# Optimization experiments

Measured on AMD Instinct MI355X. Metric: run time of the kernel, lower is better.

Reference implementation:

```python
import jax, jax.numpy as jnp
import numpy as np

B, QL, DL, RSZ, T = 16, 32, 12, 500, 2
DW, DH = 256, 512
HP = DH // 2  # per-direction GRU hidden
NW, NE = 50000, 100000


def _gru_dir(xp, mask, Wh, bh, reverse):
    # xp: [B, L, 3H'] precomputed input projections; mask: [B, L, 1]
    Hp = Wh.shape[1]
    xp_t = jnp.swapaxes(xp, 0, 1)
    m_t = jnp.swapaxes(mask, 0, 1)
    h0 = jnp.zeros((xp.shape[0], Hp), xp.dtype)

    def step(h, inp):
        x, m = inp
        gh = h @ Wh.T + bh
        r = jax.nn.sigmoid(x[:, :Hp] + gh[:, :Hp])
        z = jax.nn.sigmoid(x[:, Hp:2 * Hp] + gh[:, Hp:2 * Hp])
        n = jnp.tanh(x[:, 2 * Hp:] + r * gh[:, 2 * Hp:])
        hn = (1.0 - z) * n + z * h
        h = m * hn + (1.0 - m) * h  # skip updates at pad tokens
        return h, h

    hT, hs = jax.lax.scan(step, h0, (xp_t, m_t), reverse=reverse)
    return jnp.swapaxes(hs, 0, 1), hT


def _bigru(tokens, emb, Wx, Wh, bx, bh):
    # tokens: [B, L] int, 0 = pad. Wx: [2, 3H', D], Wh: [2, 3H', H'], bx/bh: [2, 3H']
    x = emb[tokens]
    mask = (tokens != 0).astype(x.dtype)[..., None]
    xp_f = jnp.einsum('bld,gd->blg', x, Wx[0]) + bx[0]
    xp_b = jnp.einsum('bld,gd->blg', x, Wx[1]) + bx[1]
    hs_f, hT_f = _gru_dir(xp_f, mask, Wh[0], bh[0], False)
    hs_b, hT_b = _gru_dir(xp_b, mask, Wh[1], bh[1], True)
    word_h = jnp.concatenate([hs_f, hs_b], -1) * mask  # zero pad positions
    sent = jnp.concatenate([hT_f, hT_b], -1)  # last fwd / last bwd hidden
    return word_h, sent


def setup_inputs() -> dict:
    key = jax.random.key(0)
    ks = jax.random.split(key, 12)

    def gru_p(k, din):
        k1, k2 = jax.random.split(k, 2)
        s = 1.0 / float(np.sqrt(HP))
        return (jax.random.normal(k1, (2, 3 * HP, din), jnp.float32) * s,
                jax.random.normal(k2, (2, 3 * HP, HP), jnp.float32) * s,
                jnp.zeros((2, 3 * HP), jnp.float32),
                jnp.zeros((2, 3 * HP), jnp.float32))

    q_Wx, q_Wh, q_bx, q_bh = gru_p(ks[0], DW)
    d_Wx, d_Wh, d_bx, d_bh = gru_p(ks[1], DW)
    kaim = float(np.sqrt(2.0 / DH))
    return {
        'questions': jax.random.randint(ks[2], (B, QL), 0, NW),
        'e_s': jax.random.uniform(ks[3], (B, NE), jnp.float32),
        'pair': jax.random.randint(ks[4], (T, B, RSZ, 2), 0, NE),
        'desc': jax.random.randint(ks[5], (T, B, RSZ, DL), 0, NW),
        'word_emb': jax.random.normal(ks[6], (NW, DW), jnp.float32) * 0.02,
        'q_Wx': q_Wx, 'q_Wh': q_Wh, 'q_bx': q_bx, 'q_bh': q_bh,
        'd_Wx': d_Wx, 'd_Wh': d_Wh, 'd_bx': d_bx, 'd_bh': d_bh,
        'step_W': jax.random.normal(ks[7], (T, DH, DH), jnp.float32) * kaim,
        'step_b': jnp.zeros((T, DH), jnp.float32),
        'rel_W': jax.random.normal(ks[8], (1, DH), jnp.float32) * kaim,
        'rel_b': jnp.zeros((1,), jnp.float32),
        'qcls_W': jax.random.normal(ks[9], (NE, DH), jnp.float32) * kaim,
        'qcls_b': jnp.zeros((NE,), jnp.float32),
    }


def reference(questions, e_s, pair, desc, word_emb, q_Wx, q_Wh, q_bx, q_bh,
              d_Wx, d_Wh, d_bx, d_bh, step_W, step_b, rel_W, rel_b, qcls_W, qcls_b):
    q_word_h, q_emb = _bigru(questions, word_emb, q_Wx, q_Wh, q_bx, q_bh)
    bsz, num_ent = e_s.shape
    last_e = e_s
    for t in range(pair.shape[0]):  # num_steps hops (small, fixed)
        cq = jnp.tanh(q_emb @ step_W[t].T + step_b[t])              # [B,H]
        q_dist = jax.nn.softmax(jnp.einsum('bh,blh->bl', cq, q_word_h), axis=1)
        ctx = jnp.einsum('bl,blh->bh', q_dist, q_word_h)            # [B,H]
        d_tok = desc[t].reshape(-1, desc.shape[-1])                 # [B*rsz, L]
        _, d_emb = _bigru(d_tok, word_emb, d_Wx, d_Wh, d_bx, d_bh)
        d_emb = d_emb.reshape(bsz, -1, d_emb.shape[-1])             # [B,rsz,H]
        d_logit = jnp.einsum('bh,brh,h->br', ctx, d_emb, rel_W[0]) + rel_b[0]
        d_prob = jax.nn.sigmoid(d_logit)                            # [B,rsz]
        sub, obj = pair[t, :, :, 0], pair[t, :, :, 1]
        obj_p = jnp.take_along_axis(last_e, sub, axis=1) * d_prob   # follow: gather
        last_e = jax.vmap(lambda o, p: jnp.zeros((num_ent,), e_s.dtype).at[o].add(p))(obj, obj_p)
        z = jax.lax.stop_gradient(jnp.where(last_e > 1.0, last_e, 1.0))
        last_e = last_e / z
    q_mask = jax.nn.sigmoid(q_emb @ qcls_W.T + qcls_b)
    return last_e * q_mask
```

## Files before the change

### kernel.cpp

```cpp
#include <hip/hip_runtime.h>
#include <math.h>

#define B_    16
#define QL_   32
#define DL_   12
#define RSZ_  500
#define T_    2
#define DW_   256
#define DH_   512
#define HP_   256
#define NW_   50000
#define NE_   100000
#define NSEQD (T_*B_*RSZ_)

typedef _Float16 half8 __attribute__((ext_vector_type(8)));
typedef float   floatx4 __attribute__((ext_vector_type(4)));

__device__ __forceinline__ float sigf(float x){
  return __builtin_amdgcn_rcpf(1.0f + __expf(-x));
}
__device__ __forceinline__ float tanhfast(float x){
  return 1.0f - 2.0f*__builtin_amdgcn_rcpf(1.0f + __expf(2.0f*x));
}

__global__ void k_prep_desc(const float* __restrict__ Wx, const float* __restrict__ Wh,
                            _Float16* __restrict__ Bd) {
  int i = blockIdx.x*256 + threadIdx.x;
  int dir = i / 393216;
  int rem = i % 393216;
  float v;
  if (rem < 262144) {
    int n = rem >> 9, k = rem & 511;
    v = (k < 256) ? Wx[(dir*768 + n)*256 + k] : Wh[(dir*768 + n)*256 + (k-256)];
  } else if (rem < 327680) {
    int r2 = rem - 262144; int j = r2 >> 8, k = r2 & 255;
    v = Wx[(dir*768 + 512 + j)*256 + k];
  } else {
    int r2 = rem - 327680; int j = r2 >> 8, k = r2 & 255;
    v = Wh[(dir*768 + 512 + j)*256 + k];
  }
  Bd[i] = (_Float16)v;
}

__global__ void k_prep_qwh(const float* __restrict__ Wh, _Float16* __restrict__ WhQ) {
  int i = blockIdx.x*256 + threadIdx.x;
  WhQ[i] = (_Float16)Wh[i];
}

__global__ __launch_bounds__(256) void k_xproj(
    const int* __restrict__ questions, const float* __restrict__ emb,
    const float* __restrict__ Wx, const float* __restrict__ bx,
    float* __restrict__ xp)
{
  int b = blockIdx.x, n0 = blockIdx.y*128, dir = blockIdx.z;
  int tid = threadIdx.x;
  __shared__ float As[32*256];
  {
    int l = tid >> 3, c8 = tid & 7;
    int tk = questions[b*QL_ + l];
    const float4* src = (const float4*)(emb + (size_t)tk*256) + c8*8;
    float4* dst = (float4*)(As + l*256 + c8*32);
    #pragma unroll
    for (int q = 0; q < 8; ++q) dst[q] = src[q];
  }
  __syncthreads();
  int rr = tid >> 7, jj = tid & 127;
  int n = n0 + jj;
  const float4* W4 = (const float4*)(Wx + ((size_t)dir*768 + n)*256);
  const float4* A4 = (const float4*)As;
  float acc[16];
  #pragma unroll
  for (int i = 0; i < 16; ++i) acc[i] = 0.f;
  for (int k4 = 0; k4 < 64; ++k4) {
    float4 wv = W4[k4];
    #pragma unroll
    for (int i = 0; i < 16; ++i) {
      float4 av = A4[(rr*16 + i)*64 + k4];
      acc[i] += av.x*wv.x + av.y*wv.y + av.z*wv.z + av.w*wv.w;
    }
  }
  float bias = bx[dir*768 + n];
  for (int i = 0; i < 16; ++i) {
    int l = rr*16 + i;
    xp[(((size_t)dir*QL_ + l)*16 + b)*768 + n] = acc[i] + bias;
  }
}

__global__ __launch_bounds__(1024, 4) void k_qgru(
    const int* __restrict__ questions, const _Float16* __restrict__ WhQ,
    const float* __restrict__ bh, const float* __restrict__ xp,
    float* __restrict__ qwh, float* __restrict__ qemb)
{
  const int dir = blockIdx.x;
  const int tid = threadIdx.x;
  const int lane = tid & 63, w = tid >> 6;
  const int lm = lane & 15, lq = lane >> 4;
  const int jl = w*16 + lm;

  __shared__ _Float16 hA[16*256];
  __shared__ float xpL[2][16*768];
  __shared__ int tokS[512];

  if (tid < 512) {
    tokS[tid] = questions[tid];
    int row = tid >> 5, c = tid & 31;
    half8 z8 = {0,0,0,0,0,0,0,0};
    *(half8*)(hA + row*256 + (c ^ row)*8) = z8;
  }

  const _Float16* pR = WhQ + ((size_t)dir*768 + jl)*256;
  const _Float16* pZ = WhQ + ((size_t)dir*768 + 256 + jl)*256;
  const _Float16* pG = WhQ + ((size_t)dir*768 + 512 + jl)*256;
  const float bh_r = bh[dir*768 + jl];
  const float bh_z = bh[dir*768 + 256 + jl];
  const float bh_n = bh[dir*768 + 512 + jl];
  float hreg[4] = {0.f,0.f,0.f,0.f};

  for (int t = 0; t < QL_; ++t) {
    int l = dir ? (QL_-1-t) : t;
    int par = t & 1;
    {
      const float4* src = (const float4*)(xp + (((size_t)dir*QL_ + l)*16)*768);
      float4* dst = (float4*)xpL[par];
      dst[tid]        = src[tid];
      dst[tid + 1024] = src[tid + 1024];
      dst[tid + 2048] = src[tid + 2048];
    }
    __syncthreads();

    floatx4 aR = {0,0,0,0}, aZ = {0,0,0,0}, aG = {0,0,0,0};
    #pragma unroll
    for (int kf = 0; kf < 8; ++kf) {
      int p = (kf*4 + lq) ^ lm;
      half8 a = *(const half8*)(hA + lm*256 + p*8);
      int k0 = kf*32 + lq*8;
      half8 br = *(const half8*)(pR + k0);
      half8 bz = *(const half8*)(pZ + k0);
      half8 bg = *(const half8*)(pG + k0);
      aR = __builtin_amdgcn_mfma_f32_16x16x32_f16(a, br, aR, 0,0,0);
      aZ = __builtin_amdgcn_mfma_f32_16x16x32_f16(a, bz, aZ, 0,0,0);
      aG = __builtin_amdgcn_mfma_f32_16x16x32_f16(a, bg, aG, 0,0,0);
    }
    __syncthreads();

    #pragma unroll
    for (int reg = 0; reg < 4; ++reg) {
      int b = lq*4 + reg;
      const float* xb = &xpL[par][b*768];
      float r  = sigf(xb[jl]       + aR[reg] + bh_r);
      float z  = sigf(xb[256 + jl] + aZ[reg] + bh_z);
      float nt = tanhfast(xb[512 + jl] + r*(aG[reg] + bh_n));
      float hold = hreg[reg];
      float hn = (1.f - z)*nt + z*hold;
      int tk = tokS[b*QL_ + l];
      float hnew = (tk != 0) ? hn : hold;
      hreg[reg] = hnew;
      int p2 = (jl >> 3) ^ b;
      hA[b*256 + p2*8 + (jl & 7)] = (_Float16)hnew;
      qwh[((size_t)b*QL_ + l)*512 + dir*256 + jl] = (tk != 0) ? hnew : 0.f;
    }
  }
  #pragma unroll
  for (int reg = 0; reg < 4; ++reg) {
    int b = lq*4 + reg;
    qemb[b*512 + dir*256 + jl] = hreg[reg];
  }
}

__global__ __launch_bounds__(1024, 4) void k_desc_gru(
    const int* __restrict__ desc, const float* __restrict__ emb,
    const _Float16* __restrict__ Bd, const float* __restrict__ bx,
    const float* __restrict__ bh, float* __restrict__ dh)
{
  const int dir  = blockIdx.z;
  const int seq0 = blockIdx.x * 64;
  const int tid  = threadIdx.x;
  const int lane = tid & 63, w = tid >> 6;
  const int lm = lane & 15, lq = lane >> 4;
  const int j0 = w * 16;

  __shared__ _Float16 A2[64*512];
  __shared__ int tokL[2][64];

  {
    int row = tid >> 4, cc = tid & 15;
    half8 z8 = {0,0,0,0,0,0,0,0};
    #pragma unroll
    for (int q = 0; q < 2; ++q) {
      int c = 32 + cc*2 + q;
      *(half8*)(A2 + row*512 + (c ^ row)*8) = z8;
    }
  }

  const int l0 = dir ? (DL_-1) : 0;
  const int dl = dir ? -1 : 1;

  auto stage_x = [&](int ll, int par) {
    int row = tid >> 4, cc = tid & 15;
    int s = seq0 + row;
    int tk = desc[(size_t)s*DL_ + ll];
    if (cc == 0) tokL[par][row] = tk;
    const float4* src = (const float4*)(emb + (size_t)tk*256);
    #pragma unroll
    for (int q = 0; q < 2; ++q) {
      int c = cc*2 + q;
      float4 v0 = src[c*2], v1 = src[c*2+1];
      half8 hv;
      hv[0]=(_Float16)v0.x; hv[1]=(_Float16)v0.y; hv[2]=(_Float16)v0.z; hv[3]=(_Float16)v0.w;
      hv[4]=(_Float16)v1.x; hv[5]=(_Float16)v1.y; hv[6]=(_Float16)v1.z; hv[7]=(_Float16)v1.w;
      *(half8*)(A2 + row*512 + (c ^ row)*8) = hv;
    }
  };
  stage_x(l0, 0);

  const _Float16* Bdir = Bd + (size_t)dir * 393216;
  const int jl = j0 + lm;
  const _Float16* pR = Bdir + (size_t)jl*512;
  const _Float16* pZ = Bdir + (size_t)(256 + jl)*512;
  const _Float16* pX = Bdir + 262144 + (size_t)jl*256;
  const _Float16* pG = Bdir + 327680 + (size_t)jl*256;

  const float bias_r = bx[dir*768 + jl]       + bh[dir*768 + jl];
  const float bias_z = bx[dir*768 + 256 + jl] + bh[dir*768 + 256 + jl];
  const float bias_n = bx[dir*768 + 512 + jl];
  const float bias_g = bh[dir*768 + 512 + jl];

  int l = l0;
  for (int t = 0; t < DL_; ++t, l += dl) {
    __syncthreads();

    floatx4 accR[4], accZ[4], accN[4], accG[4];
    #pragma unroll
    for (int mi = 0; mi < 4; ++mi) {
      floatx4 z4 = {0.f,0.f,0.f,0.f};
      accR[mi]=z4; accZ[mi]=z4; accN[mi]=z4; accG[mi]=z4;
    }

    #pragma unroll
    for (int half = 0; half < 2; ++half) {
      #pragma unroll 4
      for (int kk = 0; kk < 8; ++kk) {
        int kfx = half*8 + kk;
        int k0 = kfx*32 + lq*8;
        half8 br = *(const half8*)(pR + k0);
        half8 bz = *(const half8*)(pZ + k0);
        half8 bb = half ? *(const half8*)(pG + (k0 - 256))
                        : *(const half8*)(pX + k0);
        int cb = kfx*4 + lq;
        #pragma unroll
        for (int mi = 0; mi < 4; ++mi) {
          int row = mi*16 + lm;
          half8 a = *(const half8*)(A2 + row*512 + (cb ^ row)*8);
          accR[mi] = __builtin_amdgcn_mfma_f32_16x16x32_f16(a, br, accR[mi], 0,0,0);
          accZ[mi] = __builtin_amdgcn_mfma_f32_16x16x32_f16(a, bz, accZ[mi], 0,0,0);
          if (half) accG[mi] = __builtin_amdgcn_mfma_f32_16x16x32_f16(a, bb, accG[mi], 0,0,0);
          else      accN[mi] = __builtin_amdgcn_mfma_f32_16x16x32_f16(a, bb, accN[mi], 0,0,0);
        }
      }
    }

    __syncthreads();

    int par = t & 1;
    #pragma unroll
    for (int mi = 0; mi < 4; ++mi) {
      #pragma unroll
      for (int reg = 0; reg < 4; ++reg) {
        int m = mi*16 + lq*4 + reg;
        float r  = sigf(accR[mi][reg] + bias_r);
        float z  = sigf(accZ[mi][reg] + bias_z);
        float nt = tanhfast(accN[mi][reg] + bias_n + r*(accG[mi][reg] + bias_g));
        int c2 = 32 + (jl >> 3);
        _Float16* hp = A2 + m*512 + ((c2 ^ m)*8) + (jl & 7);
        float hold = (float)(*hp);
        float hn = (1.f - z)*nt + z*hold;
        int tk = tokL[par][m];
        float hnew = (tk != 0) ? hn : hold;
        *hp = (_Float16)hnew;
        if (t == DL_-1)
          dh[((size_t)dir*NSEQD + seq0 + m)*256 + jl] = hnew;
      }
    }
    if (t < DL_-1) stage_x(l + dl, (t+1) & 1);
  }
}

__global__ __launch_bounds__(256) void k_attn(
    const float* __restrict__ qemb, const float* __restrict__ qwh,
    const float* __restrict__ sW, const float* __restrict__ sb,
    const float* __restrict__ relW, float* __restrict__ u, int t)
{
  int b = blockIdx.x, tid = threadIdx.x;
  __shared__ float qe[512];
  __shared__ float cq[512];
  __shared__ float lg[32];
  __shared__ float dist[32];
  qe[tid]     = qemb[b*512 + tid];
  qe[tid+256] = qemb[b*512 + 256 + tid];
  __syncthreads();
  const float4* qe4 = (const float4*)qe;
  for (int nn = 0; nn < 2; ++nn) {
    int n = tid + nn*256;
    const float4* w4 = (const float4*)(sW + ((size_t)t*512 + n)*512);
    float acc = 0.f;
    for (int k4 = 0; k4 < 128; ++k4) {
      float4 w = w4[k4]; float4 q = qe4[k4];
      acc += w.x*q.x + w.y*q.y + w.z*q.z + w.w*q.w;
    }
    cq[n] = tanhfast(acc + sb[t*512 + n]);
  }
  __syncthreads();
  if (tid < 32) {
    const float4* r4 = (const float4*)(qwh + ((size_t)b*QL_ + tid)*512);
    const float4* c4 = (const float4*)cq;
    float acc = 0.f;
    for (int k4 = 0; k4 < 128; ++k4) {
// ... 48 lines not shown
                          const float* __restrict__ esrc, float* __restrict__ edst,
                          int t, int clampflag)
{
  int o = blockIdx.x*256 + threadIdx.x;
  if (o >= B_*RSZ_) return;
  int b = o / RSZ_, r = o % RSZ_;
  const int* pp = pair + (((size_t)t*B_ + b)*RSZ_ + r)*2;
  int sub = pp[0], obj = pp[1];
  float v = esrc[(size_t)b*NE_ + sub];
  if (clampflag) v = fminf(v, 1.0f);
  atomicAdd(edst + (size_t)b*NE_ + obj, v * dprob[o]);
}

__global__ __launch_bounds__(256) void k_final(
    const float* __restrict__ qemb, const float* __restrict__ W,
    const float* __restrict__ bias, const float* __restrict__ efin,
    float* __restrict__ out)
{
  int tid = threadIdx.x;
  int lane = tid & 63;
  int ks = lane & 15, bg = lane >> 4;
  int b = (tid >> 6)*4 + bg;
  float q[32];
  {
    const float4* q4 = (const float4*)(qemb + b*512 + ks*32);
    #pragma unroll
    for (int i = 0; i < 8; ++i) {
      float4 v = q4[i];
      q[4*i]=v.x; q[4*i+1]=v.y; q[4*i+2]=v.z; q[4*i+3]=v.w;
    }
  }
  int e0 = blockIdx.x*256;
  int eend = (e0+256 < NE_) ? e0+256 : NE_;
  for (int e = e0; e < eend; ++e) {
    const float4* w4 = (const float4*)(W + (size_t)e*512 + ks*32);
    float acc = 0.f;
    #pragma unroll
    for (int i = 0; i < 8; ++i) {
      float4 v = w4[i];
      acc += v.x*q[4*i] + v.y*q[4*i+1] + v.z*q[4*i+2] + v.w*q[4*i+3];
    }
    acc += __shfl_xor(acc, 1);
    acc += __shfl_xor(acc, 2);
    acc += __shfl_xor(acc, 4);
    acc += __shfl_xor(acc, 8);
    if (ks == 0) {
      float msk = sigf(acc + bias[e]);
      float ev = fminf(efin[(size_t)b*NE_ + e], 1.0f);
      out[(size_t)b*NE_ + e] = ev * msk;
    }
  }
}

extern "C" void kernel_launch(void* const* d_in, const int* in_sizes, int n_in,
                              void* d_out, int out_size, void* d_ws, size_t ws_size,
                              hipStream_t stream)
{
  const int*   questions = (const int*)d_in[0];
  const float* e_s   = (const float*)d_in[1];
  const int*   pair  = (const int*)d_in[2];
  const int*   desc  = (const int*)d_in[3];
  const float* emb   = (const float*)d_in[4];
  const float* qWx   = (const float*)d_in[5];
  const float* qWh   = (const float*)d_in[6];
  const float* qbx   = (const float*)d_in[7];
  const float* qbh   = (const float*)d_in[8];
  const float* dWx   = (const float*)d_in[9];
  const float* dWh   = (const float*)d_in[10];
  const float* dbx   = (const float*)d_in[11];
  const float* dbh   = (const float*)d_in[12];
  const float* stepW = (const float*)d_in[13];
  const float* stepb = (const float*)d_in[14];
  const float* relW  = (const float*)d_in[15];
  const float* relb  = (const float*)d_in[16];
  const float* qclsW = (const float*)d_in[17];
  const float* qclsb = (const float*)d_in[18];
  float* out = (float*)d_out;

  char* ws = (char*)d_ws;
  size_t off = 0;
  auto alloc = [&](size_t bytes)->void* {
    void* p = ws + off; off += (bytes + 255) & ~(size_t)255; return p;
  };
  _Float16* Bd   = (_Float16*)alloc((size_t)2*393216*sizeof(_Float16));
  _Float16* WhQ  = (_Float16*)alloc((size_t)2*768*256*sizeof(_Float16));
  float* xp   = (float*)alloc((size_t)2*QL_*16*768*sizeof(float));
  float* qemb = (float*)alloc((size_t)16*512*sizeof(float));
  float* qwh  = (float*)alloc((size_t)16*QL_*512*sizeof(float));
  float* dh   = (float*)alloc((size_t)2*NSEQD*256*sizeof(float));
  float* u    = (float*)alloc((size_t)16*512*sizeof(float));
  float* dprob= (float*)alloc((size_t)B_*RSZ_*sizeof(float));
  float* ebuf = (float*)alloc((size_t)2*B_*NE_*sizeof(float));

  hipMemsetAsync(ebuf, 0, (size_t)2*B_*NE_*sizeof(float), stream);

  k_prep_desc<<<3072, 256, 0, stream>>>(dWx, dWh, Bd);
  k_prep_qwh<<<1536, 256, 0, stream>>>(qWh, WhQ);

  k_xproj<<<dim3(16,6,2), 256, 0, stream>>>(questions, emb, qWx, qbx, xp);
  k_qgru<<<2, 1024, 0, stream>>>(questions, WhQ, qbh, xp, qwh, qemb);

  k_desc_gru<<<dim3(250,1,2), 1024, 0, stream>>>(desc, emb, Bd, dbx, dbh, dh);

  for (int t = 0; t < T_; ++t) {
    k_attn<<<16, 256, 0, stream>>>(qemb, qwh, stepW, stepb, relW, u, t);
    k_dlogit<<<2000, 256, 0, stream>>>(u, dh, relb, dprob, t);
    const float* esrc = (t == 0) ? e_s : ebuf;
    float* edst = ebuf + (size_t)t*B_*NE_;
    k_scatter<<<32, 256, 0, stream>>>(pair, dprob, esrc, edst, t, t);
  }
  k_final<<<(NE_+255)/256, 256, 0, stream>>>(qemb, qclsW, qclsb, ebuf + (size_t)B_*NE_, out);
}
```

Measured before the change: 1.821 ms.

## Fuse question and description GRUs into one launch with register-resident weights

Merges the question GRU and description GRU into a single kernel launch: 250 blocks handle description sequences (now 128 rows per block) and 2 extra blocks run the question GRU concurrently. GRU weight fragments are preloaded into registers instead of being re-read from global memory each step. The embedding table is pre-converted to fp16 once so description gathers move half the bytes, and the next step's input tokens are prefetched in registers. The entity buffer now aliases the fp16 embedding scratch and is zeroed after the fused kernel. The trade-off is very high register pressure (weights plus 32 accumulators per thread) and an extra conversion pass over the 50k×256 embedding table.

```diff
diff --git a/kernel.cpp b/kernel.cpp
--- a/kernel.cpp
+++ b/kernel.cpp
@@ -12,6 +12,9 @@
 #define NW_   50000
 #define NE_   100000
 #define NSEQD (T_*B_*RSZ_)
+#define MDESC 128
+#define NBLK_DESC 250
+#define NBLK_FUSED 252
 
 typedef _Float16 half8 __attribute__((ext_vector_type(8)));
 typedef float   floatx4 __attribute__((ext_vector_type(4)));
@@ -47,6 +50,16 @@
   WhQ[i] = (_Float16)Wh[i];
 }
 
+__global__ void k_prep_emb16(const float* __restrict__ emb, _Float16* __restrict__ emb16) {
+  int i = blockIdx.x*256 + threadIdx.x;
+  const float4* s = (const float4*)emb + (size_t)i*2;
+  float4 a = s[0], b = s[1];
+  half8 h;
+  h[0]=(_Float16)a.x; h[1]=(_Float16)a.y; h[2]=(_Float16)a.z; h[3]=(_Float16)a.w;
+  h[4]=(_Float16)b.x; h[5]=(_Float16)b.y; h[6]=(_Float16)b.z; h[7]=(_Float16)b.w;
+  *(half8*)(emb16 + (size_t)i*8) = h;
+}
+
 __global__ __launch_bounds__(256) void k_xproj(
     const int* __restrict__ questions, const float* __restrict__ emb,
     const float* __restrict__ Wx, const float* __restrict__ bx,
@@ -86,202 +99,208 @@
   }
 }
 
-__global__ __launch_bounds__(1024, 4) void k_qgru(
+__global__ __launch_bounds__(1024) void k_fused(
+    const int* __restrict__ desc, const _Float16* __restrict__ emb16,
+    const _Float16* __restrict__ Bd, const float* __restrict__ dbx,
+    const float* __restrict__ dbh, float* __restrict__ dh,
     const int* __restrict__ questions, const _Float16* __restrict__ WhQ,
-    const float* __restrict__ bh, const float* __restrict__ xp,
+    const float* __restrict__ qbh, const float* __restrict__ xp,
     float* __restrict__ qwh, float* __restrict__ qemb)
 {
-  const int dir = blockIdx.x;
+  __shared__ __align__(16) char smem[137216];
+  const int bid = blockIdx.x;
   const int tid = threadIdx.x;
   const int lane = tid & 63, w = tid >> 6;
   const int lm = lane & 15, lq = lane >> 4;
   const int jl = w*16 + lm;
 
-  __shared__ _Float16 hA[16*256];
-  __shared__ float xpL[2][16*768];
-  __shared__ int tokS[512];
-
-  if (tid < 512) {
-    tokS[tid] = questions[tid];
-    int row = tid >> 5, c = tid & 31;
-    half8 z8 = {0,0,0,0,0,0,0,0};
-    *(half8*)(hA + row*256 + (c ^ row)*8) = z8;
-  }
-
-  const _Float16* pR = WhQ + ((size_t)dir*768 + jl)*256;
-  const _Float16* pZ = WhQ + ((size_t)dir*768 + 256 + jl)*256;
-  const _Float16* pG = WhQ + ((size_t)dir*768 + 512 + jl)*256;
-  const float bh_r = bh[dir*768 + jl];
-  const float bh_z = bh[dir*768 + 256 + jl];
-  const float bh_n = bh[dir*768 + 512 + jl];
-  float hreg[4] = {0.f,0.f,0.f,0.f};
-
-  for (int t = 0; t < QL_; ++t) {
-    int l = dir ? (QL_-1-t) : t;
-    int par = t & 1;
+  if (bid < NBLK_DESC) {
+    const int dir  = (bid >= 125) ? 1 : 0;
+    const int seq0 = (bid - dir*125) * MDESC;
+    _Float16* A2   = (_Float16*)smem;
+    int*      tokA = (int*)(smem + MDESC*512*2);
+
+    for (int i = tid; i < MDESC*DL_; i += 1024)
+      tokA[i] = desc[(size_t)seq0*DL_ + i];
+
+    const int srow = tid >> 3, sp = tid & 7;
     {
-      const float4* src = (const float4*)(xp + (((size_t)dir*QL_ + l)*16)*768);
-      float4* dst = (float4*)xpL[par];
+      half8 z8 = {0,0,0,0,0,0,0,0};
+      #pragma unroll
+      for (int q = 0; q < 4; ++q) {
+        int c = 32 + sp*4 + q;
+        *(half8*)(A2 + srow*512 + ((c ^ (srow & 63))*8)) = z8;
+      }
+    }
+
+    const _Float16* Bdir = Bd + (size_t)dir*393216;
+    const _Float16* pR = Bdir + (size_t)jl*512 + lq*8;
+    const _Float16* pZ = Bdir + (size_t)(256 + jl)*512 + lq*8;
+    const _Float16* pX = Bdir + 262144 + (size_t)jl*256 + lq*8;
+    const _Float16* pG = Bdir + 327680 + (size_t)jl*256 + lq*8;
+    half8 bR[16], bZ[16], bX[8], bG[8];
+    #pragma unroll
+    for (int kt = 0; kt < 16; ++kt) {
+      bR[kt] = *(const half8*)(pR + kt*32);
+      bZ[kt] = *(const half8*)(pZ + kt*32);
+    }
+    #pragma unroll
+    for (int kt = 0; kt < 8; ++kt) {
+      bX[kt] = *(const half8*)(pX + kt*32);
+      bG[kt] = *(const half8*)(pG + kt*32);
+    }
+
+    const float bias_r = dbx[dir*768 + jl]       + dbh[dir*768 + jl];
+    const float bias_z = dbx[dir*768 + 256 + jl] + dbh[dir*768 + 256 + jl];
+    const float bias_n = dbx[dir*768 + 512 + jl];
+    const float bias_g = dbh[dir*768 + 512 + jl];
+
+    const int l0 = dir ? (DL_-1) : 0;
+    const int dl = dir ? -1 : 1;
+
+    half8 P[4];
+    auto ldx = [&](int ll) {
+      int tk = desc[(size_t)(seq0 + srow)*DL_ + ll];
+      const half8* src = (const half8*)(emb16 + (size_t)tk*256) + sp*4;
+      #pragma unroll
+      for (int q = 0; q < 4; ++q) P[q] = src[q];
+    };
+    auto stw = [&]() {
+      #pragma unroll
+      for (int q = 0; q < 4; ++q) {
+        int c = sp*4 + q;
+        *(half8*)(A2 + srow*512 + ((c ^ (srow & 63))*8)) = P[q];
+      }
+    };
+    ldx(l0); stw();
+    ldx(l0 + dl);
+    __syncthreads();
+
+    int l = l0;
+    for (int t = 0; t < DL_; ++t, l += dl) {
+      floatx4 accR[8], accZ[8], accN[8], accG[8];
+      #pragma unroll
+      for (int mi = 0; mi < 8; ++mi) {
+        floatx4 z4 = {0.f,0.f,0.f,0.f};
+        accR[mi]=z4; accZ[mi]=z4; accN[mi]=z4; accG[mi]=z4;
+      }
+      #pragma unroll
+      for (int kt = 0; kt < 16; ++kt) {
+        #pragma unroll
+        for (int mi = 0; mi < 8; ++mi) {
+          int row = mi*16 + lm;
+          half8 a = *(const half8*)(A2 + row*512 + (((kt*4 + lq) ^ (row & 63))*8));
+          accR[mi] = __builtin_amdgcn_mfma_f32_16x16x32_f16(a, bR[kt], accR[mi], 0,0,0);
+          accZ[mi] = __builtin_amdgcn_mfma_f32_16x16x32_f16(a, bZ[kt], accZ[mi], 0,0,0);
+          if (kt < 8) accN[mi] = __builtin_amdgcn_mfma_f32_16x16x32_f16(a, bX[kt],   accN[mi], 0,0,0);
+          else        accG[mi] = __builtin_amdgcn_mfma_f32_16x16x32_f16(a, bG[kt-8], accG[mi], 0,0,0);
+        }
+      }
+      __syncthreads();
+
+      #pragma unroll
+      for (int mi = 0; mi < 8; ++mi) {
+        #pragma unroll
+        for (int reg = 0; reg < 4; ++reg) {
+          int m = mi*16 + lq*4 + reg;
+          float r  = sigf(accR[mi][reg] + bias_r);
+          float z  = sigf(accZ[mi][reg] + bias_z);
+          float nt = tanhfast(accN[mi][reg] + bias_n + r*(accG[mi][reg] + bias_g));
+          int c2 = 32 + (jl >> 3);
+          _Float16* hp = A2 + m*512 + ((c2 ^ (m & 63))*8) + (jl & 7);
+          float hold = (float)(*hp);
+          float hn = (1.f - z)*nt + z*hold;
+          int tk = tokA[m*DL_ + l];
+          float hnew = (tk != 0) ? hn : hold;
+          *hp = (_Float16)hnew;
+          if (t == DL_-1)
+            dh[((size_t)dir*NSEQD + seq0 + m)*256 + jl] = hnew;
+        }
+      }
+      if (t < DL_-1) {
+        stw();
+        if (t < DL_-2) ldx(l + 2*dl);
+      }
+      __syncthreads();
+    }
+  } else {
+    const int dir = bid - NBLK_DESC;
+    _Float16* hA   = (_Float16*)smem;
+    float*    xpL  = (float*)(smem + 8192);
+    int*      tokS = (int*)(smem + 8192 + 98304);
+
+    if (tid < 512) {
+      tokS[tid] = questions[tid];
+      int row = tid >> 5, c = tid & 31;
+      half8 z8 = {0,0,0,0,0,0,0,0};
+      *(half8*)(hA + row*256 + ((c ^ row)*8)) = z8;
+    }
+
+    const _Float16* qpR = WhQ + ((size_t)dir*768 + jl)*256 + lq*8;
+    const _Float16* qpZ = WhQ + ((size_t)dir*768 + 256 + jl)*256 + lq*8;
+    const _Float16* qpG = WhQ + ((size_t)dir*768 + 512 + jl)*256 + lq*8;
+    half8 bQR[8], bQZ[8], bQG[8];
+    #pragma unroll
+    for (int kf = 0; kf < 8; ++kf) {
+      bQR[kf] = *(const half8*)(qpR + kf*32);
+      bQZ[kf] = *(const half8*)(qpZ + kf*32);
+      bQG[kf] = *(const half8*)(qpG + kf*32);
+    }
+    const float bh_r = qbh[dir*768 + jl];
+    const float bh_z = qbh[dir*768 + 256 + jl];
+    const float bh_n = qbh[dir*768 + 512 + jl];
+    float hreg[4] = {0.f,0.f,0.f,0.f};
+
+    auto stq = [&](int ll, int par) {
+      const float4* src = (const float4*)(xp + (((size_t)dir*QL_ + ll)*16)*768);
+      float4* dst = (float4*)(xpL + par*12288);
       dst[tid]        = src[tid];
       dst[tid + 1024] = src[tid + 1024];
       dst[tid + 2048] = src[tid + 2048];
-    }
+    };
+    stq(dir ? QL_-1 : 0, 0);
     __syncthreads();
 
-    floatx4 aR = {0,0,0,0}, aZ = {0,0,0,0}, aG = {0,0,0,0};
-    #pragma unroll
-    for (int kf = 0; kf < 8; ++kf) {
-      int p = (kf*4 + lq) ^ lm;
-      half8 a = *(const half8*)(hA + lm*256 + p*8);
-      int k0 = kf*32 + lq*8;
-      half8 br = *(const half8*)(pR + k0);
-      half8 bz = *(const half8*)(pZ + k0);
-      half8 bg = *(const half8*)(pG + k0);
-      aR = __builtin_amdgcn_mfma_f32_16x16x32_f16(a, br, aR, 0,0,0);
-      aZ = __builtin_amdgcn_mfma_f32_16x16x32_f16(a, bz, aZ, 0,0,0);
-      aG = __builtin_amdgcn_mfma_f32_16x16x32_f16(a, bg, aG, 0,0,0);
-    }
-    __syncthreads();
-
+    for (int t = 0; t < QL_; ++t) {
+      int l = dir ? (QL_-1-t) : t;
+      int par = t & 1;
+      if (t < QL_-1) stq(dir ? (QL_-2-t) : (t+1), par ^ 1);
+
+      floatx4 aR = {0,0,0,0}, aZ = {0,0,0,0}, aG = {0,0,0,0};
+      #pragma unroll
+      for (int kf = 0; kf < 8; ++kf) {
+        int p = (kf*4 + lq) ^ lm;
+        half8 a = *(const half8*)(hA + lm*256 + p*8);
+        aR = __builtin_amdgcn_mfma_f32_16x16x32_f16(a, bQR[kf], aR, 0,0,0);
+        aZ = __builtin_amdgcn_mfma_f32_16x16x32_f16(a, bQZ[kf], aZ, 0,0,0);
+        aG = __builtin_amdgcn_mfma_f32_16x16x32_f16(a, bQG[kf], aG, 0,0,0);
+      }
+      __syncthreads();
+
+      const float* xb0 = xpL + par*12288;
+      #pragma unroll
+      for (int reg = 0; reg < 4; ++reg) {
+        int b = lq*4 + reg;
+        const float* xb = xb0 + b*768;
+        float r  = sigf(xb[jl]       + aR[reg] + bh_r);
+        float z  = sigf(xb[256 + jl] + aZ[reg] + bh_z);
+        float nt = tanhfast(xb[512 + jl] + r*(aG[reg] + bh_n));
+        float hold = hreg[reg];
+        float hn = (1.f - z)*nt + z*hold;
+        int tk = tokS[b*QL_ + l];
+        float hnew = (tk != 0) ? hn : hold;
+        hreg[reg] = hnew;
+        int p2 = (jl >> 3) ^ b;
+        hA[b*256 + p2*8 + (jl & 7)] = (_Float16)hnew;
+        qwh[((size_t)b*QL_ + l)*512 + dir*256 + jl] = (tk != 0) ? hnew : 0.f;
+      }
+      __syncthreads();
+    }
     #pragma unroll
     for (int reg = 0; reg < 4; ++reg) {
       int b = lq*4 + reg;
-      const float* xb = &xpL[par][b*768];
-      float r  = sigf(xb[jl]       + aR[reg] + bh_r);
-      float z  = sigf(xb[256 + jl] + aZ[reg] + bh_z);
-      float nt = tanhfast(xb[512 + jl] + r*(aG[reg] + bh_n));
-      float hold = hreg[reg];
-      float hn = (1.f - z)*nt + z*hold;
-      int tk = tokS[b*QL_ + l];
-      float hnew = (tk != 0) ? hn : hold;
-      hreg[reg] = hnew;
-      int p2 = (jl >> 3) ^ b;
-      hA[b*256 + p2*8 + (jl & 7)] = (_Float16)hnew;
-      qwh[((size_t)b*QL_ + l)*512 + dir*256 + jl] = (tk != 0) ? hnew : 0.f;
-    }
-  }
-  #pragma unroll
-  for (int reg = 0; reg < 4; ++reg) {
-    int b = lq*4 + reg;
-    qemb[b*512 + dir*256 + jl] = hreg[reg];
-  }
-}
-
-__global__ __launch_bounds__(1024, 4) void k_desc_gru(
-    const int* __restrict__ desc, const float* __restrict__ emb,
-    const _Float16* __restrict__ Bd, const float* __restrict__ bx,
-    const float* __restrict__ bh, float* __restrict__ dh)
-{
-  const int dir  = blockIdx.z;
-  const int seq0 = blockIdx.x * 64;
-  const int tid  = threadIdx.x;
-  const int lane = tid & 63, w = tid >> 6;
-  const int lm = lane & 15, lq = lane >> 4;
-  const int j0 = w * 16;
-
-  __shared__ _Float16 A2[64*512];
-  __shared__ int tokL[2][64];
-
-  {
-    int row = tid >> 4, cc = tid & 15;
-    half8 z8 = {0,0,0,0,0,0,0,0};
-    #pragma unroll
-    for (int q = 0; q < 2; ++q) {
-      int c = 32 + cc*2 + q;
-      *(half8*)(A2 + row*512 + (c ^ row)*8) = z8;
-    }
-  }
-
-  const int l0 = dir ? (DL_-1) : 0;
-  const int dl = dir ? -1 : 1;
-
-  auto stage_x = [&](int ll, int par) {
-    int row = tid >> 4, cc = tid & 15;
-    int s = seq0 + row;
-    int tk = desc[(size_t)s*DL_ + ll];
-    if (cc == 0) tokL[par][row] = tk;
-    const float4* src = (const float4*)(emb + (size_t)tk*256);
-    #pragma unroll
-    for (int q = 0; q < 2; ++q) {
-      int c = cc*2 + q;
-      float4 v0 = src[c*2], v1 = src[c*2+1];
-      half8 hv;
-      hv[0]=(_Float16)v0.x; hv[1]=(_Float16)v0.y; hv[2]=(_Float16)v0.z; hv[3]=(_Float16)v0.w;
-      hv[4]=(_Float16)v1.x; hv[5]=(_Float16)v1.y; hv[6]=(_Float16)v1.z; hv[7]=(_Float16)v1.w;
-      *(half8*)(A2 + row*512 + (c ^ row)*8) = hv;
-    }
-  };
-  stage_x(l0, 0);
-
-  const _Float16* Bdir = Bd + (size_t)dir * 393216;
-  const int jl = j0 + lm;
-  const _Float16* pR = Bdir + (size_t)jl*512;
-  const _Float16* pZ = Bdir + (size_t)(256 + jl)*512;
-  const _Float16* pX = Bdir + 262144 + (size_t)jl*256;
-  const _Float16* pG = Bdir + 327680 + (size_t)jl*256;
-
-  const float bias_r = bx[dir*768 + jl]       + bh[dir*768 + jl];
-  const float bias_z = bx[dir*768 + 256 + jl] + bh[dir*768 + 256 + jl];
-  const float bias_n = bx[dir*768 + 512 + jl];
-  const float bias_g = bh[dir*768 + 512 + jl];
-
-  int l = l0;
-  for (int t = 0; t < DL_; ++t, l += dl) {
-    __syncthreads();
-
-    floatx4 accR[4], accZ[4], accN[4], accG[4];
-    #pragma unroll
-    for (int mi = 0; mi < 4; ++mi) {
-      floatx4 z4 = {0.f,0.f,0.f,0.f};
-      accR[mi]=z4; accZ[mi]=z4; accN[mi]=z4; accG[mi]=z4;
-    }
-
-    #pragma unroll
-    for (int half = 0; half < 2; ++half) {
-      #pragma unroll 4
-      for (int kk = 0; kk < 8; ++kk) {
-        int kfx = half*8 + kk;
-        int k0 = kfx*32 + lq*8;
-        half8 br = *(const half8*)(pR + k0);
-        half8 bz = *(const half8*)(pZ + k0);
-        half8 bb = half ? *(const half8*)(pG + (k0 - 256))
-                        : *(const half8*)(pX + k0);
-        int cb = kfx*4 + lq;
-        #pragma unroll
-        for (int mi = 0; mi < 4; ++mi) {
-          int row = mi*16 + lm;
-          half8 a = *(const half8*)(A2 + row*512 + (cb ^ row)*8);
-          accR[mi] = __builtin_amdgcn_mfma_f32_16x16x32_f16(a, br, accR[mi], 0,0,0);
-          accZ[mi] = __builtin_amdgcn_mfma_f32_16x16x32_f16(a, bz, accZ[mi], 0,0,0);
-          if (half) accG[mi] = __builtin_amdgcn_mfma_f32_16x16x32_f16(a, bb, accG[mi], 0,0,0);
-          else      accN[mi] = __builtin_amdgcn_mfma_f32_16x16x32_f16(a, bb, accN[mi], 0,0,0);
-        }
-      }
-    }
-
-    __syncthreads();
-
-    int par = t & 1;
-    #pragma unroll
-    for (int mi = 0; mi < 4; ++mi) {
-      #pragma unroll
-      for (int reg = 0; reg < 4; ++reg) {
-        int m = mi*16 + lq*4 + reg;
-        float r  = sigf(accR[mi][reg] + bias_r);
-        float z  = sigf(accZ[mi][reg] + bias_z);
-        float nt = tanhfast(accN[mi][reg] + bias_n + r*(accG[mi][reg] + bias_g));
-        int c2 = 32 + (jl >> 3);
-        _Float16* hp = A2 + m*512 + ((c2 ^ m)*8) + (jl & 7);
-        float hold = (float)(*hp);
-        float hn = (1.f - z)*nt + z*hold;
-        int tk = tokL[par][m];
-        float hnew = (tk != 0) ? hn : hold;
-        *hp = (_Float16)hnew;
-        if (t == DL_-1)
-          dh[((size_t)dir*NSEQD + seq0 + m)*256 + jl] = hnew;
-      }
-    }
-    if (t < DL_-1) stage_x(l + dl, (t+1) & 1);
+      qemb[b*512 + dir*256 + jl] = hreg[reg];
+    }
   }
 }
 
@@ -448,23 +467,25 @@
   };
   _Float16* Bd   = (_Float16*)alloc((size_t)2*393216*sizeof(_Float16));
   _Float16* WhQ  = (_Float16*)alloc((size_t)2*768*256*sizeof(_Float16));
+  _Float16* emb16= (_Float16*)alloc((size_t)NW_*256*sizeof(_Float16));
   float* xp   = (float*)alloc((size_t)2*QL_*16*768*sizeof(float));
   float* qemb = (float*)alloc((size_t)16*512*sizeof(float));
   float* qwh  = (float*)alloc((size_t)16*QL_*512*sizeof(float));
   float* dh   = (float*)alloc((size_t)2*NSEQD*256*sizeof(float));
   float* u    = (float*)alloc((size_t)16*512*sizeof(float));
   float* dprob= (float*)alloc((size_t)B_*RSZ_*sizeof(float));
-  float* ebuf = (float*)alloc((size_t)2*B_*NE_*sizeof(float));
-
-  hipMemsetAsync(ebuf, 0, (size_t)2*B_*NE_*sizeof(float), stream);
+  float* ebuf = (float*)emb16;
 
   k_prep_desc<<<3072, 256, 0, stream>>>(dWx, dWh, Bd);
   k_prep_qwh<<<1536, 256, 0, stream>>>(qWh, WhQ);
+  k_prep_emb16<<<6250, 256, 0, stream>>>(emb, emb16);
 
   k_xproj<<<dim3(16,6,2), 256, 0, stream>>>(questions, emb, qWx, qbx, xp);
-  k_qgru<<<2, 1024, 0, stream>>>(questions, WhQ, qbh, xp, qwh, qemb);
-
-  k_desc_gru<<<dim3(250,1,2), 1024, 0, stream>>>(desc, emb, Bd, dbx, dbh, dh);
+
+  k_fused<<<NBLK_FUSED, 1024, 0, stream>>>(desc, emb16, Bd, dbx, dbh, dh,
+                                           questions, WhQ, qbh, xp, qwh, qemb);
+
+  hipMemsetAsync(ebuf, 0, (size_t)2*B_*NE_*sizeof(float), stream);
 
   for (int t = 0; t < T_; ++t) {
     k_attn<<<16, 256, 0, stream>>>(qemb, qwh, stepW, stepb, relW, u, t);
```

New measurement: 2.461 ms. 35.1% more time.

## Fuse question and description GRUs into one launch with fp16 embedding table

Applied to the files above, without the earlier changes.

Merges the question GRU (2 blocks) and the description GRU (500 blocks) into a single kernel, so the long serial question recurrence overlaps the description work instead of running alone. The embedding table is pre-converted to fp16 once, which halves gather traffic, and the next token's embeddings are register-prefetched one step ahead. Token ids are staged in LDS up front, the question xp tile is read straight from global memory instead of through LDS, and the entity buffer aliases the fp16 table and is zeroed afterwards. The final kernel is also unrolled by two entities. The extra conversion pass over the full 50k-row table adds traffic that may offset the savings.

```diff
diff --git a/kernel.cpp b/kernel.cpp
--- a/kernel.cpp
+++ b/kernel.cpp
@@ -12,6 +12,9 @@
 #define NW_   50000
 #define NE_   100000
 #define NSEQD (T_*B_*RSZ_)
+#define MDESC 64
+#define NBLK_DESC 500
+#define NBLK_FUSED 502
 
 typedef _Float16 half8 __attribute__((ext_vector_type(8)));
 typedef float   floatx4 __attribute__((ext_vector_type(4)));
@@ -47,6 +50,16 @@
   WhQ[i] = (_Float16)Wh[i];
 }
 
+__global__ void k_prep_emb16(const float* __restrict__ emb, _Float16* __restrict__ emb16) {
+  int i = blockIdx.x*256 + threadIdx.x;
+  const float4* s = (const float4*)emb + (size_t)i*2;
+  float4 a = s[0], b = s[1];
+  half8 h;
+  h[0]=(_Float16)a.x; h[1]=(_Float16)a.y; h[2]=(_Float16)a.z; h[3]=(_Float16)a.w;
+  h[4]=(_Float16)b.x; h[5]=(_Float16)b.y; h[6]=(_Float16)b.z; h[7]=(_Float16)b.w;
+  *(half8*)(emb16 + (size_t)i*8) = h;
+}
+
 __global__ __launch_bounds__(256) void k_xproj(
     const int* __restrict__ questions, const float* __restrict__ emb,
     const float* __restrict__ Wx, const float* __restrict__ bx,
@@ -86,202 +99,204 @@
   }
 }
 
-__global__ __launch_bounds__(1024, 4) void k_qgru(
+__global__ __launch_bounds__(1024, 4) void k_fused(
+    const int* __restrict__ desc, const _Float16* __restrict__ emb16,
+    const _Float16* __restrict__ Bd, const float* __restrict__ dbx,
+    const float* __restrict__ dbh, float* __restrict__ dh,
     const int* __restrict__ questions, const _Float16* __restrict__ WhQ,
-    const float* __restrict__ bh, const float* __restrict__ xp,
+    const float* __restrict__ qbh, const float* __restrict__ xp,
     float* __restrict__ qwh, float* __restrict__ qemb)
 {
-  const int dir = blockIdx.x;
+  __shared__ __align__(16) char smem[68608];
+  const int bid = blockIdx.x;
   const int tid = threadIdx.x;
   const int lane = tid & 63, w = tid >> 6;
   const int lm = lane & 15, lq = lane >> 4;
   const int jl = w*16 + lm;
 
-  __shared__ _Float16 hA[16*256];
-  __shared__ float xpL[2][16*768];
-  __shared__ int tokS[512];
-
-  if (tid < 512) {
-    tokS[tid] = questions[tid];
-    int row = tid >> 5, c = tid & 31;
-    half8 z8 = {0,0,0,0,0,0,0,0};
-    *(half8*)(hA + row*256 + (c ^ row)*8) = z8;
-  }
-
-  const _Float16* pR = WhQ + ((size_t)dir*768 + jl)*256;
-  const _Float16* pZ = WhQ + ((size_t)dir*768 + 256 + jl)*256;
-  const _Float16* pG = WhQ + ((size_t)dir*768 + 512 + jl)*256;
-  const float bh_r = bh[dir*768 + jl];
-  const float bh_z = bh[dir*768 + 256 + jl];
-  const float bh_n = bh[dir*768 + 512 + jl];
-  float hreg[4] = {0.f,0.f,0.f,0.f};
-
-  for (int t = 0; t < QL_; ++t) {
-    int l = dir ? (QL_-1-t) : t;
-    int par = t & 1;
+  if (bid < NBLK_DESC) {
+    const int dir  = (bid >= 250) ? 1 : 0;
+    const int seq0 = (bid - dir*250) * MDESC;
+    _Float16* A2   = (_Float16*)smem;
+    int*      tokA = (int*)(smem + MDESC*512*2);
+
+    if (tid < MDESC*DL_)
+      tokA[tid] = desc[(size_t)seq0*DL_ + tid];
+
     {
-      const float4* src = (const float4*)(xp + (((size_t)dir*QL_ + l)*16)*768);
-      float4* dst = (float4*)xpL[par];
-      dst[tid]        = src[tid];
-      dst[tid + 1024] = src[tid + 1024];
-      dst[tid + 2048] = src[tid + 2048];
+      int row = tid >> 4, cc = tid & 15;
+      half8 z8 = {0,0,0,0,0,0,0,0};
+      #pragma unroll
+      for (int q = 0; q < 2; ++q) {
+        int c = 32 + cc*2 + q;
+        *(half8*)(A2 + row*512 + ((c ^ row)*8)) = z8;
+      }
     }
     __syncthreads();
 
-    floatx4 aR = {0,0,0,0}, aZ = {0,0,0,0}, aG = {0,0,0,0};
-    #pragma unroll
-    for (int kf = 0; kf < 8; ++kf) {
-      int p = (kf*4 + lq) ^ lm;
-      half8 a = *(const half8*)(hA + lm*256 + p*8);
-      int k0 = kf*32 + lq*8;
-      half8 br = *(const half8*)(pR + k0);
-      half8 bz = *(const half8*)(pZ + k0);
-      half8 bg = *(const half8*)(pG + k0);
-      aR = __builtin_amdgcn_mfma_f32_16x16x32_f16(a, br, aR, 0,0,0);
-      aZ = __builtin_amdgcn_mfma_f32_16x16x32_f16(a, bz, aZ, 0,0,0);
-      aG = __builtin_amdgcn_mfma_f32_16x16x32_f16(a, bg, aG, 0,0,0);
-    }
+    const _Float16* Bdir = Bd + (size_t)dir * 393216;
+    const _Float16* pR = Bdir + (size_t)jl*512;
+    const _Float16* pZ = Bdir + (size_t)(256 + jl)*512;
+    const _Float16* pX = Bdir + 262144 + (size_t)jl*256;
+    const _Float16* pG = Bdir + 327680 + (size_t)jl*256;
+
+    const float bias_r = dbx[dir*768 + jl]       + dbh[dir*768 + jl];
+    const float bias_z = dbx[dir*768 + 256 + jl] + dbh[dir*768 + 256 + jl];
+    const float bias_n = dbx[dir*768 + 512 + jl];
+    const float bias_g = dbh[dir*768 + 512 + jl];
+
+    const int l0 = dir ? (DL_-1) : 0;
+    const int dl = dir ? -1 : 1;
+
+    const int srow = tid >> 4, sp = tid & 15;
+    half8 P[2];
+    auto ldx = [&](int ll) {
+      int tk = tokA[srow*DL_ + ll];
+      const half8* src = (const half8*)(emb16 + (size_t)tk*256) + sp*2;
+      P[0] = __builtin_nontemporal_load(src);
+      P[1] = __builtin_nontemporal_load(src + 1);
+    };
+    auto stw = [&]() {
+      #pragma unroll
+      for (int q = 0; q < 2; ++q) {
+        int c = sp*2 + q;
+        *(half8*)(A2 + srow*512 + ((c ^ srow)*8)) = P[q];
+      }
+    };
+    ldx(l0); stw();
+    ldx(l0 + dl);
     __syncthreads();
 
+    int l = l0;
+    for (int t = 0; t < DL_; ++t, l += dl) {
+      floatx4 accR[4], accZ[4], accN[4], accG[4];
+      #pragma unroll
+      for (int mi = 0; mi < 4; ++mi) {
+        floatx4 z4 = {0.f,0.f,0.f,0.f};
+        accR[mi]=z4; accZ[mi]=z4; accN[mi]=z4; accG[mi]=z4;
+      }
+
+      #pragma unroll
+      for (int half = 0; half < 2; ++half) {
+        #pragma unroll 4
+        for (int kk = 0; kk < 8; ++kk) {
+          int kfx = half*8 + kk;
+          int k0 = kfx*32 + lq*8;
+          half8 br = *(const half8*)(pR + k0);
+          half8 bz = *(const half8*)(pZ + k0);
+          half8 bb = half ? *(const half8*)(pG + (k0 - 256))
+                          : *(const half8*)(pX + k0);
+          int cb = kfx*4 + lq;
+          #pragma unroll
+          for (int mi = 0; mi < 4; ++mi) {
+            int row = mi*16 + lm;
+            half8 a = *(const half8*)(A2 + row*512 + ((cb ^ row)*8));
+            accR[mi] = __builtin_amdgcn_mfma_f32_16x16x32_f16(a, br, accR[mi], 0,0,0);
+            accZ[mi] = __builtin_amdgcn_mfma_f32_16x16x32_f16(a, bz, accZ[mi], 0,0,0);
+            if (half) accG[mi] = __builtin_amdgcn_mfma_f32_16x16x32_f16(a, bb, accG[mi], 0,0,0);
+            else      accN[mi] = __builtin_amdgcn_mfma_f32_16x16x32_f16(a, bb, accN[mi], 0,0,0);
+          }
+        }
+      }
+
+      __syncthreads();
+
+      #pragma unroll
+      for (int mi = 0; mi < 4; ++mi) {
+        #pragma unroll
+        for (int reg = 0; reg < 4; ++reg) {
+          int m = mi*16 + lq*4 + reg;
+          float r  = sigf(accR[mi][reg] + bias_r);
+          float z  = sigf(accZ[mi][reg] + bias_z);
+          float nt = tanhfast(accN[mi][reg] + bias_n + r*(accG[mi][reg] + bias_g));
+          int c2 = 32 + (jl >> 3);
+          _Float16* hp = A2 + m*512 + ((c2 ^ m)*8) + (jl & 7);
+          float hold = (float)(*hp);
+          float hn = (1.f - z)*nt + z*hold;
+          int tk = tokA[m*DL_ + l];
+          float hnew = (tk != 0) ? hn : hold;
+          *hp = (_Float16)hnew;
+          if (t == DL_-1)
+            dh[((size_t)dir*NSEQD + seq0 + m)*256 + jl] = hnew;
+        }
+      }
+      if (t < DL_-1) {
+        stw();
+        if (t < DL_-2) ldx(l + 2*dl);
+      }
+      __syncthreads();
+    }
+  } else {
+    const int dir = bid - NBLK_DESC;
+    _Float16* hA   = (_Float16*)smem;
+    int*      tokS = (int*)(smem + 65536);
+
+    if (tid < 512) {
+      tokS[tid] = questions[tid];
+      int row = tid >> 5, c = tid & 31;
+      half8 z8 = {0,0,0,0,0,0,0,0};
+      *(half8*)(hA + row*256 + ((c ^ row)*8)) = z8;
+    }
+    __syncthreads();
+
+    const _Float16* pR = WhQ + ((size_t)dir*768 + jl)*256;
+    const _Float16* pZ = WhQ + ((size_t)dir*768 + 256 + jl)*256;
+    const _Float16* pG = WhQ + ((size_t)dir*768 + 512 + jl)*256;
+    const float bh_r = qbh[dir*768 + jl];
+    const float bh_z = qbh[dir*768 + 256 + jl];
+    const float bh_n = qbh[dir*768 + 512 + jl];
+    float hreg[4] = {0.f,0.f,0.f,0.f};
+
+    for (int t = 0; t < QL_; ++t) {
+      int l = dir ? (QL_-1-t) : t;
+
+      float xr[4], xz[4], xn[4];
+      #pragma unroll
+      for (int reg = 0; reg < 4; ++reg) {
+        int b = lq*4 + reg;
+        const float* xb = xp + (((size_t)dir*QL_ + l)*16 + b)*768;
+        xr[reg] = xb[jl];
+        xz[reg] = xb[256 + jl];
+        xn[reg] = xb[512 + jl];
+      }
+
+      floatx4 aR = {0,0,0,0}, aZ = {0,0,0,0}, aG = {0,0,0,0};
+      #pragma unroll
+      for (int kf = 0; kf < 8; ++kf) {
+        int p = (kf*4 + lq) ^ lm;
+        half8 a = *(const half8*)(hA + lm*256 + p*8);
+        int k0 = kf*32 + lq*8;
+        half8 br = *(const half8*)(pR + k0);
+        half8 bz = *(const half8*)(pZ + k0);
+        half8 bg = *(const half8*)(pG + k0);
+        aR = __builtin_amdgcn_mfma_f32_16x16x32_f16(a, br, aR, 0,0,0);
+        aZ = __builtin_amdgcn_mfma_f32_16x16x32_f16(a, bz, aZ, 0,0,0);
+        aG = __builtin_amdgcn_mfma_f32_16x16x32_f16(a, bg, aG, 0,0,0);
+      }
+      __syncthreads();
+
+      #pragma unroll
+      for (int reg = 0; reg < 4; ++reg) {
+        int b = lq*4 + reg;
+        float r  = sigf(xr[reg] + aR[reg] + bh_r);
+        float z  = sigf(xz[reg] + aZ[reg] + bh_z);
+        float nt = tanhfast(xn[reg] + r*(aG[reg] + bh_n));
+        float hold = hreg[reg];
+        float hn = (1.f - z)*nt + z*hold;
+        int tk = tokS[b*QL_ + l];
+        float hnew = (tk != 0) ? hn : hold;
+        hreg[reg] = hnew;
+        int p2 = (jl >> 3) ^ b;
+        hA[b*256 + p2*8 + (jl & 7)] = (_Float16)hnew;
+        qwh[((size_t)b*QL_ + l)*512 + dir*256 + jl] = (tk != 0) ? hnew : 0.f;
+      }
+      __syncthreads();
+    }
     #pragma unroll
     for (int reg = 0; reg < 4; ++reg) {
       int b = lq*4 + reg;
-      const float* xb = &xpL[par][b*768];
-      float r  = sigf(xb[jl]       + aR[reg] + bh_r);
-      float z  = sigf(xb[256 + jl] + aZ[reg] + bh_z);
-      float nt = tanhfast(xb[512 + jl] + r*(aG[reg] + bh_n));
-      float hold = hreg[reg];
-      float hn = (1.f - z)*nt + z*hold;
-      int tk = tokS[b*QL_ + l];
-      float hnew = (tk != 0) ? hn : hold;
-      hreg[reg] = hnew;
-      int p2 = (jl >> 3) ^ b;
-      hA[b*256 + p2*8 + (jl & 7)] = (_Float16)hnew;
-      qwh[((size_t)b*QL_ + l)*512 + dir*256 + jl] = (tk != 0) ? hnew : 0.f;
-    }
-  }
-  #pragma unroll
-  for (int reg = 0; reg < 4; ++reg) {
-    int b = lq*4 + reg;
-    qemb[b*512 + dir*256 + jl] = hreg[reg];
-  }
-}
-
-__global__ __launch_bounds__(1024, 4) void k_desc_gru(
-    const int* __restrict__ desc, const float* __restrict__ emb,
-    const _Float16* __restrict__ Bd, const float* __restrict__ bx,
-    const float* __restrict__ bh, float* __restrict__ dh)
-{
-  const int dir  = blockIdx.z;
-  const int seq0 = blockIdx.x * 64;
-  const int tid  = threadIdx.x;
-  const int lane = tid & 63, w = tid >> 6;
-  const int lm = lane & 15, lq = lane >> 4;
-  const int j0 = w * 16;
-
-  __shared__ _Float16 A2[64*512];
-  __shared__ int tokL[2][64];
-
-  {
-    int row = tid >> 4, cc = tid & 15;
-    half8 z8 = {0,0,0,0,0,0,0,0};
-    #pragma unroll
-    for (int q = 0; q < 2; ++q) {
-      int c = 32 + cc*2 + q;
-      *(half8*)(A2 + row*512 + (c ^ row)*8) = z8;
-    }
-  }
-
-  const int l0 = dir ? (DL_-1) : 0;
-  const int dl = dir ? -1 : 1;
-
-  auto stage_x = [&](int ll, int par) {
-    int row = tid >> 4, cc = tid & 15;
-    int s = seq0 + row;
-    int tk = desc[(size_t)s*DL_ + ll];
-    if (cc == 0) tokL[par][row] = tk;
-    const float4* src = (const float4*)(emb + (size_t)tk*256);
-    #pragma unroll
-    for (int q = 0; q < 2; ++q) {
-      int c = cc*2 + q;
-      float4 v0 = src[c*2], v1 = src[c*2+1];
-      half8 hv;
-      hv[0]=(_Float16)v0.x; hv[1]=(_Float16)v0.y; hv[2]=(_Float16)v0.z; hv[3]=(_Float16)v0.w;
-      hv[4]=(_Float16)v1.x; hv[5]=(_Float16)v1.y; hv[6]=(_Float16)v1.z; hv[7]=(_Float16)v1.w;
-      *(half8*)(A2 + row*512 + (c ^ row)*8) = hv;
-    }
-  };
-  stage_x(l0, 0);
-
-  const _Float16* Bdir = Bd + (size_t)dir * 393216;
-  const int jl = j0 + lm;
-  const _Float16* pR = Bdir + (size_t)jl*512;
-  const _Float16* pZ = Bdir + (size_t)(256 + jl)*512;
-  const _Float16* pX = Bdir + 262144 + (size_t)jl*256;
-  const _Float16* pG = Bdir + 327680 + (size_t)jl*256;
-
-  const float bias_r = bx[dir*768 + jl]       + bh[dir*768 + jl];
-  const float bias_z = bx[dir*768 + 256 + jl] + bh[dir*768 + 256 + jl];
-  const float bias_n = bx[dir*768 + 512 + jl];
-  const float bias_g = bh[dir*768 + 512 + jl];
-
-  int l = l0;
-  for (int t = 0; t < DL_; ++t, l += dl) {
-    __syncthreads();
-
-    floatx4 accR[4], accZ[4], accN[4], accG[4];
-    #pragma unroll
-    for (int mi = 0; mi < 4; ++mi) {
-      floatx4 z4 = {0.f,0.f,0.f,0.f};
-      accR[mi]=z4; accZ[mi]=z4; accN[mi]=z4; accG[mi]=z4;
-    }
-
-    #pragma unroll
-    for (int half = 0; half < 2; ++half) {
-      #pragma unroll 4
-      for (int kk = 0; kk < 8; ++kk) {
-        int kfx = half*8 + kk;
-        int k0 = kfx*32 + lq*8;
-        half8 br = *(const half8*)(pR + k0);
-        half8 bz = *(const half8*)(pZ + k0);
-        half8 bb = half ? *(const half8*)(pG + (k0 - 256))
-                        : *(const half8*)(pX + k0);
-        int cb = kfx*4 + lq;
-        #pragma unroll
-        for (int mi = 0; mi < 4; ++mi) {
-          int row = mi*16 + lm;
-          half8 a = *(const half8*)(A2 + row*512 + (cb ^ row)*8);
-          accR[mi] = __builtin_amdgcn_mfma_f32_16x16x32_f16(a, br, accR[mi], 0,0,0);
-          accZ[mi] = __builtin_amdgcn_mfma_f32_16x16x32_f16(a, bz, accZ[mi], 0,0,0);
-          if (half) accG[mi] = __builtin_amdgcn_mfma_f32_16x16x32_f16(a, bb, accG[mi], 0,0,0);
-          else      accN[mi] = __builtin_amdgcn_mfma_f32_16x16x32_f16(a, bb, accN[mi], 0,0,0);
-        }
-      }
-    }
-
-    __syncthreads();
-
-    int par = t & 1;
-    #pragma unroll
-    for (int mi = 0; mi < 4; ++mi) {
-      #pragma unroll
-      for (int reg = 0; reg < 4; ++reg) {
-        int m = mi*16 + lq*4 + reg;
-        float r  = sigf(accR[mi][reg] + bias_r);
-        float z  = sigf(accZ[mi][reg] + bias_z);
-        float nt = tanhfast(accN[mi][reg] + bias_n + r*(accG[mi][reg] + bias_g));
-        int c2 = 32 + (jl >> 3);
-        _Float16* hp = A2 + m*512 + ((c2 ^ m)*8) + (jl & 7);
-        float hold = (float)(*hp);
-        float hn = (1.f - z)*nt + z*hold;
-        int tk = tokL[par][m];
-        float hnew = (tk != 0) ? hn : hold;
-        *hp = (_Float16)hnew;
-        if (t == DL_-1)
-          dh[((size_t)dir*NSEQD + seq0 + m)*256 + jl] = hnew;
-      }
-    }
-    if (t < DL_-1) stage_x(l + dl, (t+1) & 1);
+      qemb[b*512 + dir*256 + jl] = hreg[reg];
+    }
   }
 }
 
@@ -396,22 +411,28 @@
   }
   int e0 = blockIdx.x*256;
   int eend = (e0+256 < NE_) ? e0+256 : NE_;
-  for (int e = e0; e < eend; ++e) {
-    const float4* w4 = (const float4*)(W + (size_t)e*512 + ks*32);
-    float acc = 0.f;
+  for (int e = e0; e < eend; e += 2) {
+    const float4* w4a = (const float4*)(W + (size_t)e*512 + ks*32);
+    const float4* w4b = (const float4*)(W + (size_t)(e+1)*512 + ks*32);
+    float acca = 0.f, accb = 0.f;
     #pragma unroll
     for (int i = 0; i < 8; ++i) {
-      float4 v = w4[i];
-      acc += v.x*q[4*i] + v.y*q[4*i+1] + v.z*q[4*i+2] + v.w*q[4*i+3];
-    }
-    acc += __shfl_xor(acc, 1);
-    acc += __shfl_xor(acc, 2);
-    acc += __shfl_xor(acc, 4);
-    acc += __shfl_xor(acc, 8);
+      float4 va = w4a[i];
+      float4 vb = w4b[i];
+      acca += va.x*q[4*i] + va.y*q[4*i+1] + va.z*q[4*i+2] + va.w*q[4*i+3];
+      accb += vb.x*q[4*i] + vb.y*q[4*i+1] + vb.z*q[4*i+2] + vb.w*q[4*i+3];
+    }
+    acca += __shfl_xor(acca, 1); accb += __shfl_xor(accb, 1);
+    acca += __shfl_xor(acca, 2); accb += __shfl_xor(accb, 2);
+    acca += __shfl_xor(acca, 4); accb += __shfl_xor(accb, 4);
+    acca += __shfl_xor(acca, 8); accb += __shfl_xor(accb, 8);
     if (ks == 0) {
-      float msk = sigf(acc + bias[e]);
-      float ev = fminf(efin[(size_t)b*NE_ + e], 1.0f);
-      out[(size_t)b*NE_ + e] = ev * msk;
+      float mska = sigf(acca + bias[e]);
+      float eva  = fminf(efin[(size_t)b*NE_ + e], 1.0f);
+      out[(size_t)b*NE_ + e] = eva * mska;
+      float mskb = sigf(accb + bias[e+1]);
+      float evb  = fminf(efin[(size_t)b*NE_ + e+1], 1.0f);
+      out[(size_t)b*NE_ + e+1] = evb * mskb;
     }
   }
 }
@@ -448,23 +469,25 @@
   };
   _Float16* Bd   = (_Float16*)alloc((size_t)2*393216*sizeof(_Float16));
   _Float16* WhQ  = (_Float16*)alloc((size_t)2*768*256*sizeof(_Float16));
+  _Float16* emb16= (_Float16*)alloc((size_t)NW_*256*sizeof(_Float16));
   float* xp   = (float*)alloc((size_t)2*QL_*16*768*sizeof(float));
   float* qemb = (float*)alloc((size_t)16*512*sizeof(float));
   float* qwh  = (float*)alloc((size_t)16*QL_*512*sizeof(float));
   float* dh   = (float*)alloc((size_t)2*NSEQD*256*sizeof(float));
   float* u    = (float*)alloc((size_t)16*512*sizeof(float));
   float* dprob= (float*)alloc((size_t)B_*RSZ_*sizeof(float));
-  float* ebuf = (float*)alloc((size_t)2*B_*NE_*sizeof(float));
-
-  hipMemsetAsync(ebuf, 0, (size_t)2*B_*NE_*sizeof(float), stream);
+  float* ebuf = (float*)emb16;
 
   k_prep_desc<<<3072, 256, 0, stream>>>(dWx, dWh, Bd);
   k_prep_qwh<<<1536, 256, 0, stream>>>(qWh, WhQ);
+  k_prep_emb16<<<6250, 256, 0, stream>>>(emb, emb16);
 
   k_xproj<<<dim3(16,6,2), 256, 0, stream>>>(questions, emb, qWx, qbx, xp);
-  k_qgru<<<2, 1024, 0, stream>>>(questions, WhQ, qbh, xp, qwh, qemb);
-
-  k_desc_gru<<<dim3(250,1,2), 1024, 0, stream>>>(desc, emb, Bd, dbx, dbh, dh);
+
+  k_fused<<<NBLK_FUSED, 1024, 0, stream>>>(desc, emb16, Bd, dbx, dbh, dh,
+                                           questions, WhQ, qbh, xp, qwh, qemb);
+
+  hipMemsetAsync(ebuf, 0, (size_t)2*B_*NE_*sizeof(float), stream);
 
   for (int t = 0; t < T_; ++t) {
     k_attn<<<16, 256, 0, stream>>>(qemb, qwh, stepW, stepb, relW, u, t);
```

Result: faster. 1.766 ms (-3.0%).
